# Kernel tuning notes

Hardware: AMD Instinct MI355X
Metric: run time of the kernel (lower is better)

The kernel has to match this reference:

```python
import jax, jax.numpy as jnp
import numpy as np

NUM_HEADS = 16
HEAD_DIM = 64
SCALE = 1.0 / np.sqrt(HEAD_DIM).astype(np.float32)


def _clinear(xr, xi, wr, wi):
    # complex matmul: (xr + i xi) @ (wr + i wi)
    yr = jnp.dot(xr, wr) - jnp.dot(xi, wi)
    yi = jnp.dot(xr, wi) + jnp.dot(xi, wr)
    return yr, yi


def setup_inputs() -> dict:
    key = jax.random.key(0)
    ks = jax.random.split(key, 12)
    B, L, S, C = 2, 2048, 2048, 1024
    glorot = 1.0 / np.sqrt(C)
    inp = {
        'inputs_real': jax.random.normal(ks[0], (B, L, C), jnp.float32),
        'inputs_imag': jax.random.normal(ks[1], (B, L, C), jnp.float32),
        'context_real': jax.random.normal(ks[2], (B, S, C), jnp.float32),
        'context_imag': jax.random.normal(ks[3], (B, S, C), jnp.float32),
        'wq_r': jax.random.normal(ks[4], (C, C), jnp.float32) * glorot,
        'wq_i': jax.random.normal(ks[5], (C, C), jnp.float32) * glorot,
        'wk_r': jax.random.normal(ks[6], (C, C), jnp.float32) * glorot,
        'wk_i': jax.random.normal(ks[7], (C, C), jnp.float32) * glorot,
        'wv_r': jax.random.normal(ks[8], (C, C), jnp.float32) * glorot,
        'wv_i': jax.random.normal(ks[9], (C, C), jnp.float32) * glorot,
        'wo_r': jax.random.normal(ks[10], (C, C), jnp.float32) * glorot,
        'wo_i': jax.random.normal(ks[11], (C, C), jnp.float32) * glorot,
        'bo_r': jnp.zeros((C,), jnp.float32),
        'bo_i': jnp.zeros((C,), jnp.float32),
    }
    return inp


def reference(inputs_real, inputs_imag, context_real, context_imag,
              wq_r, wq_i, wk_r, wk_i, wv_r, wv_i, wo_r, wo_i, bo_r, bo_i):
    B, L, C = inputs_real.shape
    S = context_real.shape[1]
    H, D = NUM_HEADS, HEAD_DIM

    qr, qi = _clinear(inputs_real, inputs_imag, wq_r, wq_i)
    kr, ki = _clinear(context_real, context_imag, wk_r, wk_i)
    vr, vi = _clinear(context_real, context_imag, wv_r, wv_i)

    qr = qr.reshape(B, L, H, D); qi = qi.reshape(B, L, H, D)
    kr = kr.reshape(B, S, H, D); ki = ki.reshape(B, S, H, D)
    vr = vr.reshape(B, S, H, D); vi = vi.reshape(B, S, H, D)

    # real part of q . conj-free inner product: qr.kr + qi.ki, scaled
    scores = (jnp.einsum('blhd,bshd->bhls', qr, kr)
              + jnp.einsum('blhd,bshd->bhls', qi, ki)) * SCALE
    attn = jax.nn.softmax(scores, axis=-1)

    out_r = jnp.einsum('bhls,bshd->blhd', attn, vr).reshape(B, L, C)
    out_i = jnp.einsum('bhls,bshd->blhd', attn, vi).reshape(B, L, C)

    yr, yi = _clinear(out_r, out_i, wo_r, wo_i)
    yr = yr + bo_r
    yi = yi + bo_i
    # stack real/imag parts: shape [2, B, L, C]
    return jnp.stack([yr, yi], axis=0)
```

## Files before the change

kernel.cpp:

```cpp
#include <hip/hip_runtime.h>

#define BB 2
#define LQ 2048
#define SK 2048
#define CH 1024
#define NH 16
#define HD 64
#define GK 2048
#define MM 4096
#define ATT_SCALE 0.125f

typedef _Float16 f16x8 __attribute__((ext_vector_type(8)));
typedef float f32x4 __attribute__((ext_vector_type(4)));
typedef unsigned short u16x8 __attribute__((ext_vector_type(8)));

__device__ __forceinline__ unsigned short h2u(_Float16 h) {
    union { _Float16 h; unsigned short u; } v; v.h = h; return v.u;
}
__device__ __forceinline__ void gload16(const _Float16* g, unsigned short* l) {
    __builtin_amdgcn_global_load_lds(
        (const __attribute__((address_space(1))) void*)g,
        (__attribute__((address_space(3))) void*)l, 16, 0, 0);
}

__device__ __forceinline__ float dpp_max16(float x) {
    union { float f; int i; } v, r;
    v.f = x;
    r.i = __builtin_amdgcn_update_dpp(v.i, v.i, 0xB1, 0xF, 0xF, false);
    v.f = fmaxf(v.f, r.f);
    r.i = __builtin_amdgcn_update_dpp(v.i, v.i, 0x4E, 0xF, 0xF, false);
    v.f = fmaxf(v.f, r.f);
    r.i = __builtin_amdgcn_update_dpp(v.i, v.i, 0x141, 0xF, 0xF, false);
    v.f = fmaxf(v.f, r.f);
    r.i = __builtin_amdgcn_update_dpp(v.i, v.i, 0x140, 0xF, 0xF, false);
    v.f = fmaxf(v.f, r.f);
    return v.f;
}

struct PackXEnt { const float* r; const float* i; _Float16* dst; };
struct PackXBatch { PackXEnt e[2]; };

__global__ __launch_bounds__(256) void pack_x_kernel(PackXBatch b)
{
    PackXEnt e = b.e[blockIdx.z];
    const size_t total = (size_t)MM * GK;
    for (size_t idx = (size_t)blockIdx.x * 256 + threadIdx.x; idx < total;
         idx += (size_t)gridDim.x * 256) {
        size_t m = idx >> 11;
        int c = (int)(idx & 2047);
        float v = (c < CH) ? e.r[m * CH + c] : e.i[m * CH + (c - CH)];
        e.dst[idx] = (_Float16)v;
    }
}

struct PackWEnt { const float* a; const float* b; float signb; _Float16* dst; };
struct PackWBatch { PackWEnt e[8]; };

__global__ __launch_bounds__(256) void pack_w_kernel(PackWBatch bt)
{
    PackWEnt e = bt.e[blockIdx.z];
    const int k0 = blockIdx.x * 32;
    const int n0 = blockIdx.y * 32;
    const float* src = (k0 < CH) ? e.a : e.b;
    const float sign = (k0 < CH) ? 1.f : e.signb;
    const int kk = k0 & (CH - 1);

    __shared__ float sT[32][33];
    const int t = threadIdx.x;
    const int tx = t & 31, ty = t >> 5;

    #pragma unroll
    for (int r = 0; r < 4; r++) {
        int kl = ty + r * 8;
        sT[kl][tx] = src[(size_t)(kk + kl) * CH + n0 + tx] * sign;
    }
    __syncthreads();
    #pragma unroll
    for (int r = 0; r < 4; r++) {
        int nl = ty + r * 8;
        e.dst[(size_t)(n0 + nl) * GK + k0 + tx] = (_Float16)sT[tx][nl];
    }
}

struct GemmEnt { const _Float16* A; const _Float16* Bt; void* out;
                 const float* bias; int mode; int part; };
struct GemmBatch { GemmEnt e[6]; };

__global__ __launch_bounds__(256) void mfma_cgemm(GemmBatch bt)
{
    GemmEnt e = bt.e[blockIdx.z];
    __shared__ unsigned short sA[128 * 32];
    __shared__ unsigned short sB[128 * 32];

    const int t = threadIdx.x;
    const int wave = t >> 6;
    const int lane = t & 63;
    const int wm = (wave >> 1) * 64;
    const int wn = (wave & 1) * 64;
    const int lm = lane & 15;
    const int quad = lane >> 4;

    const int m0 = blockIdx.y * 128;
    const int n0 = blockIdx.x * 128;

    const int srow = t >> 2;
    const int sseg = (t & 3) * 8;
    const _Float16* ga = e.A + (size_t)(m0 + srow) * GK + sseg;
    const _Float16* gb = e.Bt + (size_t)(n0 + srow) * GK + sseg;
    unsigned short* la = sA + t * 8;
    unsigned short* lb = sB + t * 8;

    f32x4 acc[4][4] = {};

    for (int k0 = 0; k0 < GK; k0 += 32) {
        gload16(ga + k0, la);
        gload16(ga + k0 + (size_t)64 * GK, la + 64 * 32);
        gload16(gb + k0, lb);
        gload16(gb + k0 + (size_t)64 * GK, lb + 64 * 32);
        __syncthreads();

        f16x8 af[4], bfr[4];
        #pragma unroll
        for (int i = 0; i < 4; i++)
            af[i] = *(const f16x8*)&sA[(wm + i * 16 + lm) * 32 + quad * 8];
        #pragma unroll
        for (int j = 0; j < 4; j++)
            bfr[j] = *(const f16x8*)&sB[(wn + j * 16 + lm) * 32 + quad * 8];
        #pragma unroll
        for (int i = 0; i < 4; i++)
            #pragma unroll
            for (int j = 0; j < 4; j++)
                acc[i][j] = __builtin_amdgcn_mfma_f32_16x16x32_f16(
                    af[i], bfr[j], acc[i][j], 0, 0, 0);
        __syncthreads();
    }

    const int mode = e.mode, part = e.part;
    #pragma unroll
    for (int j = 0; j < 4; j++) {
        int gcol = n0 + wn + j * 16 + lm;
        float bv = (mode == 2 && e.bias) ? e.bias[gcol] : 0.f;
        #pragma unroll
        for (int i = 0; i < 4; i++) {
            int growb = m0 + wm + i * 16 + quad * 4;
            #pragma unroll
            for (int reg = 0; reg < 4; reg++) {
                int grow = growb + reg;
                float v = acc[i][j][reg];
                if (mode == 2) {
                    ((float*)e.out)[(size_t)grow * CH + gcol] = v + bv;
                } else {
                    int b = grow >> 11, l = grow & 2047;
                    int h = gcol >> 6, dd = gcol & 63;
                    size_t off;
                    if (mode == 0)
                        off = (((size_t)(b * NH + h)) * LQ + l) * 128 + part * 64 + dd;
                    else
                        off = (((size_t)(b * NH + h)) * 128 + part * 64 + dd) * SK + l;
                    ((_Float16*)e.out)[off] = (_Float16)v;
                }
            }
        }
    }
}

#define KSTR 136
#define PSTR 72

__global__ __launch_bounds__(256, 2) void attn_mfma(
    const _Float16* __restrict__ Qp, const _Float16* __restrict__ Kp,
    const _Float16* __restrict__ Vt, _Float16* __restrict__ Aattn)
{
    __shared__ unsigned short lds[28288];
    unsigned short* sP = lds;
    unsigned short* sK = lds + 9216;
    unsigned short* sV = lds + 17920;

    const int t    = threadIdx.x;
    const int w    = t >> 6;
    const int lane = t & 63;
    const int lm   = lane & 15;
    const int quad = lane >> 4;

    const int bid = blockIdx.x;
    const int mt  = bid & 15;
    const int h   = (bid >> 4) & 15;
    const int b   = bid >> 8;

    const _Float16* qb = Qp + (((size_t)(b * NH + h)) * LQ + (size_t)mt * 128) * 128;
    const _Float16* kb = Kp + ((size_t)(b * NH + h)) * SK * 128;
    const _Float16* vb = Vt + ((size_t)(b * NH + h)) * 128 * SK;

    #pragma unroll
    for (int p = 0; p < 8; p++) {
        int idx = p * 256 + t;
        int r = idx >> 4, sg = idx & 15;
        *(u16x8*)&lds[r * KSTR + sg * 8] = *(const u16x8*)(qb + (size_t)r * 128 + sg * 8);
    }
    for (int idx = t; idx < 16 * PSTR; idx += 256) {
        sV[128 * PSTR + idx] = 0x3C00;
    }
    __syncthreads();

    f16x8 qf[2][4];
    #pragma unroll
    for (int i = 0; i < 2; i++)
        #pragma unroll
        for (int kk = 0; kk < 4; kk++)
            qf[i][kk] = *(const f16x8*)&lds[(w * 32 + i * 16 + lm) * KSTR + kk * 32 + quad * 8];

    u16x8 kreg[4], vreg[4];
    #pragma unroll
    for (int p = 0; p < 4; p++) {
        int idx = p * 256 + t;
        int r = idx >> 4, sg = idx & 15;
        kreg[p] = *(const u16x8*)(kb + (size_t)r * 128 + sg * 8);
        int rv = idx >> 3, sv = idx & 7;
        vreg[p] = *(const u16x8*)(vb + (size_t)rv * SK + sv * 8);
    }

    f32x4 oacc[2][9] = {};
    float m_st[2][4];
    #pragma unroll
    for (int i = 0; i < 2; i++)
        #pragma unroll
        for (int r = 0; r < 4; r++) m_st[i][r] = -1e30f;

    const float SC2 = ATT_SCALE * 1.44269504f;

    for (int it = 0; it < SK / 64; ++it) {
        __syncthreads();
        #pragma unroll
        for (int p = 0; p < 4; p++) {
            int idx = p * 256 + t;
            int r = idx >> 4, sg = idx & 15;
            *(u16x8*)&sK[r * KSTR + sg * 8] = kreg[p];
            int rv = idx >> 3, sv = idx & 7;
            *(u16x8*)&sV[rv * PSTR + sv * 8] = vreg[p];
        }
        __syncthreads();

        if (it + 1 < SK / 64) {
            int s0n = (it + 1) * 64;
            #pragma unroll
            for (int p = 0; p < 4; p++) {
                int idx = p * 256 + t;
                int r = idx >> 4, sg = idx & 15;
                kreg[p] = *(const u16x8*)(kb + (size_t)(s0n + r) * 128 + sg * 8);
                int rv = idx >> 3, sv = idx & 7;
                vreg[p] = *(const u16x8*)(vb + (size_t)rv * SK + s0n + sv * 8);
            }
        }

        f32x4 sacc[2][4] = {};
        #pragma unroll
        for (int kk = 0; kk < 4; kk++) {
            f16x8 bfr[4];
            #pragma unroll
            for (int j = 0; j < 4; j++)
                bfr[j] = *(const f16x8*)&sK[(j * 16 + lm) * KSTR + kk * 32 + quad * 8];
            #pragma unroll
            for (int i = 0; i < 2; i++)
                #pragma unroll
                for (int j = 0; j < 4; j++)
                    sacc[i][j] = __builtin_amdgcn_mfma_f32_16x16x32_f16(
                        qf[i][kk], bfr[j], sacc[i][j], 0, 0, 0);
        }

        #pragma unroll
        for (int i = 0; i < 2; i++) {
            #pragma unroll
            for (int r = 0; r < 4; r++) {
                float mx = fmaxf(fmaxf(sacc[i][0][r], sacc[i][1][r]),
                                 fmaxf(sacc[i][2][r], sacc[i][3][r]));
                mx = dpp_max16(mx) * SC2;
                float mnew = fmaxf(m_st[i][r], mx);
                float al = exp2f(m_st[i][r] - mnew);
                m_st[i][r] = mnew;
                int prow = (w * 32 + i * 16 + quad * 4 + r) * PSTR;
                #pragma unroll
                for (int j = 0; j < 4; j++) {
                    float p = exp2f(sacc[i][j][r] * SC2 - mnew);
                    sP[prow + j * 16 + lm] = h2u((_Float16)p);
                }
                #pragma unroll
                for (int j2 = 0; j2 < 9; j2++)
                    oacc[i][j2][r] *= al;
            }
        }

        #pragma unroll
        for (int kk = 0; kk < 2; kk++) {
            f16x8 pf[2], vf[9];
            #pragma unroll
            for (int i = 0; i < 2; i++)
                pf[i] = *(const f16x8*)&sP[(w * 32 + i * 16 + lm) * PSTR + kk * 32 + quad * 8];
            #pragma unroll
            for (int j2 = 0; j2 < 9; j2++)
                vf[j2] = *(const f16x8*)&sV[(j2 * 16 + lm) * PSTR + kk * 32 + quad * 8];
            #pragma unroll
            for (int i = 0; i < 2; i++)
                #pragma unroll
                for (int j2 = 0; j2 < 9; j2++)
                    oacc[i][j2] = __builtin_amdgcn_mfma_f32_16x16x32_f16(
                        pf[i], vf[j2], oacc[i][j2], 0, 0, 0);
        }
    }

    #pragma unroll
    for (int i = 0; i < 2; i++) {
        #pragma unroll
        for (int r = 0; r < 4; r++) {
            float inv = 1.f / oacc[i][8][r];
            int ml = w * 32 + i * 16 + quad * 4 + r;
            size_t row = (size_t)b * LQ + (size_t)mt * 128 + ml;
            #pragma unroll
            for (int j2 = 0; j2 < 8; j2++) {
                int d = j2 * 16 + lm;
                int dcol = (d < HD) ? h * HD + d : CH + h * HD + (d - HD);
                Aattn[row * GK + dcol] = (_Float16)(oacc[i][j2][r] * inv);
            }
        }
    }
}

extern "C" void kernel_launch(void* const* d_in, const int* in_sizes, int n_in,
                              void* d_out, int out_size, void* d_ws, size_t ws_size,
                              hipStream_t stream)
{
    const float* in_r = (const float*)d_in[0];
    const float* in_i = (const float*)d_in[1];
    const float* cx_r = (const float*)d_in[2];
    const float* cx_i = (const float*)d_in[3];
    const float* wq_r = (const float*)d_in[4];
    const float* wq_i = (const float*)d_in[5];
    const float* wk_r = (const float*)d_in[6];
    const float* wk_i = (const float*)d_in[7];
    const float* wv_r = (const float*)d_in[8];
    const float* wv_i = (const float*)d_in[9];
    const float* wo_r = (const float*)d_in[10];
    const float* wo_i = (const float*)d_in[11];
    const float* bo_r = (const float*)d_in[12];
    const float* bo_i = (const float*)d_in[13];

    _Float16* ws = (_Float16*)d_ws;
    const size_t A_ELEMS = (size_t)MM * GK;
    const size_t B_ELEMS = (size_t)CH * GK;
    const size_t H_ELEMS = (size_t)BB * NH * LQ * 128;

    _Float16* Ain   = ws;
    _Float16* Aattn = ws;
    _Float16* Actx  = Ain + A_ELEMS;
    _Float16* Bp    = Actx + A_ELEMS;
    _Float16* Qp    = Bp + 8 * B_ELEMS;
    _Float16* Kp    = Qp + H_ELEMS;
    _Float16* Vt    = Kp + H_ELEMS;

    _Float16* Bq_r = Bp + 0 * B_ELEMS;
    _Float16* Bq_i = Bp + 1 * B_ELEMS;
    _Float16* Bk_r = Bp + 2 * B_ELEMS;
    _Float16* Bk_i = Bp + 3 * B_ELEMS;
    _Float16* Bv_r = Bp + 4 * B_ELEMS;
    _Float16* Bv_i = Bp + 5 * B_ELEMS;
    _Float16* Bo_r = Bp + 6 * B_ELEMS;
    _Float16* Bo_i = Bp + 7 * B_ELEMS;

    float* out = (float*)d_out;
    float* yr = out;
    float* yi = out + (size_t)MM * CH;

    PackXBatch px;
    px.e[0] = { in_r, in_i, Ain  };
    px.e[1] = { cx_r, cx_i, Actx };
    pack_x_kernel<<<dim3(4096, 1, 2), 256, 0, stream>>>(px);

    PackWBatch pw;
    pw.e[0] = { wq_r, wq_i, -1.f, Bq_r };
    pw.e[1] = { wq_i, wq_r,  1.f, Bq_i };
    pw.e[2] = { wk_r, wk_i, -1.f, Bk_r };
    pw.e[3] = { wk_i, wk_r,  1.f, Bk_i };
    pw.e[4] = { wv_r, wv_i, -1.f, Bv_r };
    pw.e[5] = { wv_i, wv_r,  1.f, Bv_i };
    pw.e[6] = { wo_r, wo_i, -1.f, Bo_r };
    pw.e[7] = { wo_i, wo_r,  1.f, Bo_i };
    pack_w_kernel<<<dim3(GK / 32, CH / 32, 8), 256, 0, stream>>>(pw);

    GemmBatch gq;
    gq.e[0] = { Ain,  Bq_r, Qp, nullptr, 0, 0 };
    gq.e[1] = { Ain,  Bq_i, Qp, nullptr, 0, 1 };
    gq.e[2] = { Actx, Bk_r, Kp, nullptr, 0, 0 };
    gq.e[3] = { Actx, Bk_i, Kp, nullptr, 0, 1 };
    gq.e[4] = { Actx, Bv_r, Vt, nullptr, 1, 0 };
    gq.e[5] = { Actx, Bv_i, Vt, nullptr, 1, 1 };
    mfma_cgemm<<<dim3(CH / 128, MM / 128, 6), 256, 0, stream>>>(gq);

    attn_mfma<<<dim3(BB * NH * (LQ / 128)), 256, 0, stream>>>(Qp, Kp, Vt, Aattn);

    GemmBatch go;
    go.e[0] = { Aattn, Bo_r, yr, bo_r, 2, 0 };
    go.e[1] = { Aattn, Bo_i, yi, bo_i, 2, 1 };
    for (int z = 2; z < 6; z++) go.e[z] = go.e[0];
    mfma_cgemm<<<dim3(CH / 128, MM / 128, 2), 256, 0, stream>>>(go);
}
```

Baseline: 513.5 us.

## Pipeline GEMM with 4-stage LDS ring, swizzle, and 256x128 tiles

After: 486.7 us. 1.06x faster.

```diff
diff --git a/kernel.cpp b/kernel.cpp
--- a/kernel.cpp
+++ b/kernel.cpp
@@ -86,63 +86,97 @@
                  const float* bias; int mode; int part; };
 struct GemmBatch { GemmEnt e[6]; };
 
-__global__ __launch_bounds__(256) void mfma_cgemm(GemmBatch bt)
+#define NT   (GK / 32)
+#define BUFH 12288
+
+#define SWZ(x) ((x) ^ ((((x) >> 7) & 3) << 4))
+
+__global__ __launch_bounds__(512, 2) void mfma_cgemm(GemmBatch bt)
 {
     GemmEnt e = bt.e[blockIdx.z];
-    __shared__ unsigned short sA[128 * 32];
-    __shared__ unsigned short sB[128 * 32];
-
-    const int t = threadIdx.x;
+    __shared__ unsigned short lds[4 * BUFH];
+
+    const int t    = threadIdx.x;
     const int wave = t >> 6;
     const int lane = t & 63;
-    const int wm = (wave >> 1) * 64;
-    const int wn = (wave & 1) * 64;
-    const int lm = lane & 15;
+    const int lm   = lane & 15;
     const int quad = lane >> 4;
-
-    const int m0 = blockIdx.y * 128;
+    const int wr   = wave >> 1;
+    const int wc   = wave & 1;
+
+    const int m0 = blockIdx.y * 256;
     const int n0 = blockIdx.x * 128;
 
-    const int srow = t >> 2;
-    const int sseg = (t & 3) * 8;
-    const _Float16* ga = e.A + (size_t)(m0 + srow) * GK + sseg;
-    const _Float16* gb = e.Bt + (size_t)(n0 + srow) * GK + sseg;
-    unsigned short* la = sA + t * 8;
-    unsigned short* lb = sB + t * 8;
+    int srow[2], scol[2];
+    #pragma unroll
+    for (int L = 0; L < 2; L++) {
+        int p = (L * 512 + t) * 16;
+        int q = SWZ(p);
+        srow[L] = q >> 6;
+        scol[L] = (q >> 1) & 31;
+    }
+
+    const _Float16* gA = e.A  + (size_t)m0 * GK;
+    const _Float16* gB = e.Bt + (size_t)n0 * GK;
+
+    auto stage = [&](int kt) {
+        unsigned short* base = lds + (kt & 3) * BUFH;
+        #pragma unroll
+        for (int L = 0; L < 2; L++)
+            gload16(gA + (size_t)srow[L] * GK + kt * 32 + scol[L],
+                    base + (L * 512 + t) * 8);
+        gload16(gB + (size_t)srow[0] * GK + kt * 32 + scol[0],
+                base + 8192 + t * 8);
+    };
+
+    const int qA    = (wr * 64 + lm) * 64 + quad * 16;
+    const int physA = SWZ(qA) >> 1;
+    const int qB    = (wc * 64 + lm) * 64 + quad * 16;
+    const int physB = (SWZ(qB) >> 1) + 8192;
 
     f32x4 acc[4][4] = {};
 
-    for (int k0 = 0; k0 < GK; k0 += 32) {
-        gload16(ga + k0, la);
-        gload16(ga + k0 + (size_t)64 * GK, la + 64 * 32);
-        gload16(gb + k0, lb);
-        gload16(gb + k0 + (size_t)64 * GK, lb + 64 * 32);
-        __syncthreads();
-
-        f16x8 af[4], bfr[4];
+    stage(0); stage(1); stage(2);
+    asm volatile("s_waitcnt vmcnt(6)" ::: "memory");
+    __builtin_amdgcn_s_barrier();
+
+    for (int kt = 0; kt < NT; ++kt) {
+        const unsigned short* buf = lds + (kt & 3) * BUFH;
+        f16x8 af[4], bf[4];
         #pragma unroll
         for (int i = 0; i < 4; i++)
-            af[i] = *(const f16x8*)&sA[(wm + i * 16 + lm) * 32 + quad * 8];
+            af[i] = *(const f16x8*)&buf[physA + i * 512];
         #pragma unroll
         for (int j = 0; j < 4; j++)
-            bfr[j] = *(const f16x8*)&sB[(wn + j * 16 + lm) * 32 + quad * 8];
+            bf[j] = *(const f16x8*)&buf[physB + j * 512];
+
+        if (kt + 3 < NT) stage(kt + 3);
+
+        __builtin_amdgcn_s_barrier();
+        asm volatile("s_waitcnt lgkmcnt(0)" ::: "memory");
+        __builtin_amdgcn_s_setprio(1);
         #pragma unroll
         for (int i = 0; i < 4; i++)
             #pragma unroll
             for (int j = 0; j < 4; j++)
                 acc[i][j] = __builtin_amdgcn_mfma_f32_16x16x32_f16(
-                    af[i], bfr[j], acc[i][j], 0, 0, 0);
-        __syncthreads();
+                    af[i], bf[j], acc[i][j], 0, 0, 0);
+        __builtin_amdgcn_s_setprio(0);
+
+        if (kt < NT - 3)       asm volatile("s_waitcnt vmcnt(6)" ::: "memory");
+        else if (kt == NT - 3) asm volatile("s_waitcnt vmcnt(3)" ::: "memory");
+        else if (kt == NT - 2) asm volatile("s_waitcnt vmcnt(0)" ::: "memory");
+        __builtin_amdgcn_s_barrier();
     }
 
     const int mode = e.mode, part = e.part;
     #pragma unroll
     for (int j = 0; j < 4; j++) {
-        int gcol = n0 + wn + j * 16 + lm;
+        int gcol = n0 + wc * 64 + j * 16 + lm;
         float bv = (mode == 2 && e.bias) ? e.bias[gcol] : 0.f;
         #pragma unroll
         for (int i = 0; i < 4; i++) {
-            int growb = m0 + wm + i * 16 + quad * 4;
+            int growb = m0 + wr * 64 + i * 16 + quad * 4;
             #pragma unroll
             for (int reg = 0; reg < 4; reg++) {
                 int grow = growb + reg;
@@ -392,7 +426,7 @@
     gq.e[3] = { Actx, Bk_i, Kp, nullptr, 0, 1 };
     gq.e[4] = { Actx, Bv_r, Vt, nullptr, 1, 0 };
     gq.e[5] = { Actx, Bv_i, Vt, nullptr, 1, 1 };
-    mfma_cgemm<<<dim3(CH / 128, MM / 128, 6), 256, 0, stream>>>(gq);
+    mfma_cgemm<<<dim3(CH / 128, MM / 256, 6), 512, 0, stream>>>(gq);
 
     attn_mfma<<<dim3(BB * NH * (LQ / 128)), 256, 0, stream>>>(Qp, Kp, Vt, Aattn);
 
@@ -400,5 +434,5 @@
     go.e[0] = { Aattn, Bo_r, yr, bo_r, 2, 0 };
     go.e[1] = { Aattn, Bo_i, yi, bo_i, 2, 1 };
     for (int z = 2; z < 6; z++) go.e[z] = go.e[0];
-    mfma_cgemm<<<dim3(CH / 128, MM / 128, 2), 256, 0, stream>>>(go);
-}
+    mfma_cgemm<<<dim3(CH / 128, MM / 256, 2), 512, 0, stream>>>(go);
+}
```
